# Optimization experiments

Hardware: AMD Instinct MI355X
Metric: run time of the kernel (lower is better)

The kernel has to match this reference:

```python
import jax, jax.numpy as jnp
import numpy as np

B, HS, WS = 4, 64, 64
UP = 8
H, W = HS * UP, WS * UP
C_ORI, C_MNT, C_OFF = 90, 180, 8
K = 1024            # max minutiae candidates per image (64*64 cells max 4096)
THRESH = 0.5
DIST_T = 16.0
ANG_T = np.pi / 6


def setup_inputs() -> dict:
    key = jax.random.key(0)
    ks = jax.random.split(key, 8)
    return {
        'segmentation': jax.random.uniform(ks[0], (B, 1, HS, WS), jnp.float32),
        'segmentation_up': jax.random.uniform(ks[1], (B, 1, H, W), jnp.float32),
        'orientation_up': jax.random.normal(ks[2], (B, C_ORI, H, W), jnp.float32),
        'enhanced_real': jax.random.normal(ks[3], (B, 1, H, W), jnp.float32),
        'minutiae_score': jax.random.uniform(ks[4], (B, 1, HS, WS), jnp.float32),
        'minutiae_orientation': jax.random.normal(ks[5], (B, C_MNT, HS, WS), jnp.float32),
        'minutiae_x_offset': jax.random.normal(ks[6], (B, C_OFF, HS, WS), jnp.float32),
        'minutiae_y_offset': jax.random.normal(ks[7], (B, C_OFF, HS, WS), jnp.float32),
    }


def _opening(x, k):
    # morphological opening (erosion then dilation) with a k x k ones kernel,
    # separable min/max pooling; geodesic border (pad so border is neutral).
    pl, pr = (k - 1) // 2, k // 2

    def pool(v, comp, init, pad_val):
        vp = jnp.pad(v, ((0, 0), (pl, pr), (pl, pr)), constant_values=pad_val)
        vp = jax.lax.reduce_window(vp, init, comp, (1, k, 1), (1, 1, 1), 'VALID')
        return jax.lax.reduce_window(vp, init, comp, (1, 1, k), (1, 1, 1), 'VALID')

    er = pool(x, jax.lax.min, np.inf, 1e4)
    return pool(er, jax.lax.max, -np.inf, -1e4)


def _nms_keep(xy, ang, valid):
    # xy: [K,2], ang: [K], valid: [K] bool; entries already sorted by score desc
    d = jnp.sqrt(jnp.sum((xy[:, None, :] - xy[None, :, :]) ** 2, axis=-1))
    da = jnp.abs(ang[:, None] - ang[None, :])
    da = jnp.minimum(da, 2 * jnp.pi - da)
    sup = (d < DIST_T) & (da < ANG_T) & valid[:, None] & valid[None, :]
    idxs = jnp.arange(K)

    def body(i, keep):
        return keep & ~(sup[i] & (idxs > i) & keep[i])

    return jax.lax.fori_loop(0, K, body, valid)


def _detect(score, ori, xo, yo):
    # score: [HS,WS]; ori: [C_MNT,HS,WS]; xo/yo: [C_OFF,HS,WS]
    h, w = score.shape
    flat = score.reshape(-1)
    masked = jnp.where(flat > THRESH, flat, -1.0)
    vals, idx = jax.lax.top_k(masked, K)          # sorted descending
    valid = vals > THRESH
    rows = idx // w
    cols = idx % w
    ang_idx = jnp.argmax(ori.reshape(C_MNT, -1)[:, idx], axis=0)
    xoff = jnp.argmax(xo.reshape(C_OFF, -1)[:, idx], axis=0)
    yoff = jnp.argmax(yo.reshape(C_OFF, -1)[:, idx], axis=0)
    angles = (ang_idx.astype(jnp.float32) * 2.0 - 89.0) * (np.pi / 180.0)
    xc = cols.astype(jnp.float32) * 8.0 + xoff.astype(jnp.float32)
    yc = rows.astype(jnp.float32) * 8.0 + yoff.astype(jnp.float32)
    scores = flat[idx]
    m = jnp.stack([xc, yc, angles, scores], axis=-1)  # [K,4]
    keep = _nms_keep(m[:, :2], angles, valid)
    return m, keep


def reference(segmentation, segmentation_up, orientation_up, enhanced_real,
              minutiae_score, minutiae_orientation, minutiae_x_offset,
              minutiae_y_offset):
    mask = _opening(jnp.round(segmentation[:, 0]), 5)          # [B,HS,WS]
    mask_up = _opening(jnp.round(segmentation_up[:, 0]), 5 * UP)  # [B,H,W]

    score = minutiae_score[:, 0] * mask
    minut, keep = jax.vmap(_detect)(score, minutiae_orientation,
                                    minutiae_x_offset, minutiae_y_offset)
    minut = minut * keep[..., None].astype(minut.dtype)       # zero suppressed

    ori_field = (jnp.argmax(orientation_up, axis=1).astype(jnp.float32) * 2.0
                 - 90.0) * (np.pi / 180.0) * mask_up

    enh = enhanced_real[:, 0] * mask_up
    ef = enh.reshape(B, -1)
    emin = ef.min(axis=1, keepdims=True)
    emax = ef.max(axis=1, keepdims=True)
    enh_vis = ((ef - emin) / (emax - emin + 1e-8)).reshape(B, H, W) * 255.0

    return (minut, keep.astype(jnp.float32), enh_vis, mask_up * 255.0, ori_field)
```

## Files before the change

### kernel.cpp

```cpp
#include <hip/hip_runtime.h>
#include <math.h>

#define Hh 512
#define Wh 512
#define Bn 4
#define C_ORIc 90
#define C_MNTc 180
#define C_OFFc 8
#define Kc 1024

#define O_MINUT 0
#define O_KEEP  (Bn*Kc*4)
#define O_VIS   (O_KEEP + Bn*Kc)
#define O_MASK  (O_VIS + Bn*Hh*Wh)
#define O_ORI   (O_MASK + Bn*Hh*Wh)

#define PI_180 0.017453292519943295f
#define TWO_PI 6.283185307179586f
#define ANG_T  0.5235987755982988f

#define IMG    262144
#define PB     (256*Bn)

__device__ __forceinline__ unsigned enc_f(float f) {
    unsigned u = __float_as_uint(f);
    return (u & 0x80000000u) ? ~u : (u | 0x80000000u);
}
__device__ __forceinline__ float dec_f(unsigned e) {
    return __uint_as_float((e & 0x80000000u) ? (e ^ 0x80000000u) : ~e);
}

template <bool ISMIN, bool BIN>
__device__ __forceinline__ void vert_pass_body(const float* __restrict__ in,
                                               float* __restrict__ outp, int blk)
{
    const float SENT = ISMIN ? 1e30f : -1e30f;
    int b  = blk >> 8;
    int rg = (blk >> 3) & 31;
    int cg = blk & 7;
    int tx = threadIdx.x & 63, ty = threadIdx.x >> 6;
    int c  = cg * 64 + tx;
    int r0 = rg * 16 + ty * 4;
    const float* p = in + (size_t)b * IMG + c;

    #define LDV(rr) (((rr) >= 0 && (rr) < 512) ? (BIN ? rintf(p[(rr) * 512]) \
                                                      : p[(rr) * 512]) : SENT)
    #define OPV(a, bb) (ISMIN ? fminf(a, bb) : fmaxf(a, bb))
    float core = SENT;
    #pragma unroll
    for (int k = 0; k < 37; k++) core = OPV(core, LDV(r0 - 16 + k));
    float L2v = LDV(r0 - 17);
    float L1v = OPV(LDV(r0 - 18), L2v);
    float L0v = OPV(LDV(r0 - 19), L1v);
    float H1v = LDV(r0 + 21);
    float H2v = OPV(H1v, LDV(r0 + 22));
    float H3v = OPV(H2v, LDV(r0 + 23));
    float* q = outp + (size_t)b * IMG + (size_t)r0 * 512 + c;
    q[0]    = OPV(core, L0v);
    q[512]  = OPV(core, OPV(L1v, H1v));
    q[1024] = OPV(core, OPV(L2v, H2v));
    q[1536] = OPV(core, H3v);
    #undef LDV
    #undef OPV
}

__global__ __launch_bounds__(256) void k1_vert_erode_detect(
    const float* __restrict__ segup, const float* __restrict__ mscore,
    const float* __restrict__ seg, const float* __restrict__ mo,
    const float* __restrict__ xo, const float* __restrict__ yo,
    float* __restrict__ out, float* __restrict__ T1, unsigned* __restrict__ mmu)
{
    __shared__ union {
        unsigned long long keys[4096];
        float scr[8320];
    } U;
    __shared__ unsigned smBits[128];
    __shared__ unsigned short smHalf[256];

    int tid = threadIdx.x;
    if (blockIdx.x < PB) {
        vert_pass_body<true, true>(segup, T1, blockIdx.x);
        return;
    }

    int b = blockIdx.x - PB;
    if (tid == 0) { mmu[b * 2] = 0xFFFFFFFFu; mmu[b * 2 + 1] = 0u; }

    const float* sg = seg + b * 4096;
    float* scr0 = U.scr;
    float* scr1 = U.scr + 4160;
    for (int i = tid; i < 4096; i += 256)
        scr0[(i >> 6) * 65 + (i & 63)] = rintf(sg[i]);
    __syncthreads();
    for (int i = tid; i < 4096; i += 256) {
        int r = i >> 6, c = i & 63;
        int lo = max(r - 2, 0), hi = min(r + 2, 63);
        float m = 1e30f;
        for (int rr = lo; rr <= hi; rr++) m = fminf(m, scr0[rr * 65 + c]);
        scr1[r * 65 + c] = m;
    }
    __syncthreads();
    for (int i = tid; i < 4096; i += 256) {
        int r = i >> 6, c = i & 63;
        int lo = max(c - 2, 0), hi = min(c + 2, 63);
        float m = 1e30f;
        for (int cc = lo; cc <= hi; cc++) m = fminf(m, scr1[r * 65 + cc]);
        scr0[r * 65 + c] = m;
    }
    __syncthreads();
    for (int i = tid; i < 4096; i += 256) {
        int r = i >> 6, c = i & 63;
        int lo = max(r - 2, 0), hi = min(r + 2, 63);
        float m = -1e30f;
        for (int rr = lo; rr <= hi; rr++) m = fmaxf(m, scr0[rr * 65 + c]);
        scr1[r * 65 + c] = m;
    }
    __syncthreads();
    {
        unsigned short bits16 = 0;
        int i0 = tid * 16;
        int r = i0 >> 6;
        for (int j = 0; j < 16; j++) {
            int c = (i0 + j) & 63;
            int lo = max(c - 2, 0), hi = min(c + 2, 63);
            float m = -1e30f;
            for (int cc = lo; cc <= hi; cc++) m = fmaxf(m, scr1[r * 65 + cc]);
            bits16 |= ((unsigned short)(m != 0.0f)) << j;
        }
        smHalf[tid] = bits16;
    }
    __syncthreads();
    if (tid < 128)
        smBits[tid] = (unsigned)smHalf[2 * tid] | ((unsigned)smHalf[2 * tid + 1] << 16);
    __syncthreads();

    const float* sp = mscore + b * 4096;
    bool anyv = false;
    for (int i = tid; i < 4096; i += 256) {
        unsigned m = (smBits[i >> 5] >> (i & 31)) & 1u;
        anyv |= (m && sp[i] > 0.5f);
    }
    if (!__syncthreads_or(anyv)) {
        float4 z = {0.f, 0.f, 0.f, 0.f};
        float4* mo4 = (float4*)(out + O_MINUT + (size_t)b * 4096);
        for (int i = tid; i < 1024; i += 256) mo4[i] = z;
        ((float4*)(out + O_KEEP + (size_t)b * 1024))[tid] = z;
        return;
    }

    for (int i = tid; i < 4096; i += 256) {
        unsigned m = (smBits[i >> 5] >> (i & 31)) & 1u;
        float s = m ? sp[i] : 0.0f;
        float mval = (s > 0.5f) ? s : -1.0f;
        unsigned fb = __float_as_uint(mval);
        unsigned od = (fb & 0x80000000u) ? ~fb : (fb | 0x80000000u);
        U.keys[i] = ((unsigned long long)(~od) << 32) | (unsigned)i;
    }
    for (int k = 2; k <= 4096; k <<= 1) {
        for (int j = k >> 1; j > 0; j >>= 1) {
            __syncthreads();
            for (int t = tid; t < 4096; t += 256) {
                int ixj = t ^ j;
                if (ixj > t) {
                    unsigned long long va = U.keys[t], vb = U.keys[ixj];
                    bool up = ((t & k) == 0);
                    if ((va > vb) == up) { U.keys[t] = vb; U.keys[ixj] = va; }
                }
            }
        }
    }
    __syncthreads();

    int idxs[4]; float ss[4]; int vld[4];
    int Nv = 0;
    for (int j = 0; j < 4; j++) {
        int slot = tid + j * 256;
        int idx = (int)(U.keys[slot] & 0xffffffffu);
        unsigned m = (smBits[idx >> 5] >> (idx & 31)) & 1u;
        float s = m ? sp[idx] : 0.0f;
        idxs[j] = idx; ss[j] = s; vld[j] = (s > 0.5f);
        Nv += __syncthreads_count(vld[j]);
    }

    float xcs[4], ycs[4], angs[4];
    for (int j = 0; j < 4; j++) {
        int slot = tid + j * 256;
        xcs[j] = ycs[j] = angs[j] = 0.f;
        if (slot < Nv) {
            int idx = idxs[j];
            int rr = idx >> 6, cc = idx & 63;
            const float* op_ = mo + (size_t)b * C_MNTc * 4096 + idx;
            float best = op_[0]; int bi = 0;
            for (int ch = 1; ch < C_MNTc; ch++) {
                float v = op_[ch * 4096];
                if (v > best) { best = v; bi = ch; }
            }
            const float* xp = xo + (size_t)b * C_OFFc * 4096 + idx;
            float bxv = xp[0]; int bx = 0;
            for (int ch = 1; ch < C_OFFc; ch++) {
                float v = xp[ch * 4096];
                if (v > bxv) { bxv = v; bx = ch; }
            }
            const float* yp = yo + (size_t)b * C_OFFc * 4096 + idx;
            float byv = yp[0]; int by = 0;
            for (int ch = 1; ch < C_OFFc; ch++) {
                float v = yp[ch * 4096];
                if (v > byv) { byv = v; by = ch; }
            }
            angs[j] = ((float)bi * 2.0f - 89.0f) * PI_180;
            xcs[j]  = (float)cc * 8.0f + (float)bx;
            ycs[j]  = (float)rr * 8.0f + (float)by;
        }
    }
    __syncthreads();
    float* sx = U.scr;
    float* sy = U.scr + 1024;
    float* sa = U.scr + 2048;
    int*   keep = (int*)(U.scr + 3072);
    for (int j = 0; j < 4; j++) {
        int slot = tid + j * 256;
        sx[slot] = xcs[j]; sy[slot] = ycs[j]; sa[slot] = angs[j];
        keep[slot] = (slot < Nv) ? 1 : 0;
    }
    __syncthreads();

    for (int i = 0; i < Nv; i++) {
        if (keep[i]) {
            float xi = sx[i], yi = sy[i], ai = sa[i];
            for (int j = 0; j < 4; j++) {
                int slot = tid + j * 256;
                if (slot > i && slot < Nv && keep[slot]) {
                    float dx = xcs[j] - xi, dy = ycs[j] - yi;
                    float d = sqrtf(dx * dx + dy * dy);
                    float da = fabsf(angs[j] - ai);
                    da = fminf(da, TWO_PI - da);
                    if (d < 16.0f && da < ANG_T) keep[slot] = 0;
                }
            }
        }
        __syncthreads();
    }
    for (int j = 0; j < 4; j++) {
        int slot = tid + j * 256;
        int kf = keep[slot];
        float* mout = out + O_MINUT + (size_t)b * 4096 + slot * 4;
        if (kf) {
            mout[0] = xcs[j]; mout[1] = ycs[j]; mout[2] = angs[j]; mout[3] = ss[j];
        } else {
            mout[0] = 0.f; mout[1] = 0.f; mout[2] = 0.f; mout[3] = 0.f;
        }
        out[O_KEEP + b * 1024 + slot] = (float)kf;
    }
}

__global__ __launch_bounds__(512) void k2_horiz_erode(const float* __restrict__ T1,
                                                      float* __restrict__ T2)
{
    __shared__ float row[4][512];
    int b = blockIdx.y;
    int r0 = blockIdx.x * 4;
    int tx = threadIdx.x, ty = threadIdx.y;
    const float* p = T1 + (size_t)b * IMG + (size_t)(r0 + ty) * 512;
    ((float4*)row[ty])[tx] = ((const float4*)p)[tx];
    __syncthreads();
    int c0 = tx * 4;
    const float* rw = row[ty];
    #define LDH(cc) (((cc) >= 0 && (cc) < 512) ? rw[cc] : 1e30f)
    float core = 1e30f;
    #pragma unroll
    for (int k = 0; k < 37; k++) core = fminf(core, LDH(c0 - 16 + k));
    float L2v = LDH(c0 - 17);
    float L1v = fminf(LDH(c0 - 18), L2v);
    float L0v = fminf(LDH(c0 - 19), L1v);
    float H1v = LDH(c0 + 21);
    float H2v = fminf(H1v, LDH(c0 + 22));
    float H3v = fminf(H2v, LDH(c0 + 23));
    #undef LDH
    float4 o;
    o.x = fminf(core, L0v);
    o.y = fminf(core, fminf(L1v, H1v));
    o.z = fminf(core, fminf(L2v, H2v));
    o.w = fminf(core, H3v);
    ((float4*)(T2 + (size_t)b * IMG + (size_t)(r0 + ty) * 512))[tx] = o;
}

__global__ __launch_bounds__(256) void k3_vert_dilate(const float* __restrict__ T2,
                                                      float* __restrict__ T3)
{
    vert_pass_body<false, false>(T2, T3, blockIdx.x);
}

__global__ __launch_bounds__(512) void k4_final(const float* __restrict__ T3,
                                                const float* __restrict__ ori,
                                                const float* __restrict__ enh,
                                                float* __restrict__ out,
                                                unsigned* __restrict__ mmu)
{
    __shared__ float row[4][512];
    __shared__ float red[512];
    int b = blockIdx.y;
    int r0 = blockIdx.x * 4;
    int tx = threadIdx.x, ty = threadIdx.y;
    int ltid = ty * 128 + tx;
    const float* p = T3 + (size_t)b * IMG + (size_t)(r0 + ty) * 512;
    ((float4*)row[ty])[tx] = ((const float4*)p)[tx];
    __syncthreads();
    int c0 = tx * 4;
    const float* rw = row[ty];
    #define LDD(cc) (((cc) >= 0 && (cc) < 512) ? rw[cc] : -1e30f)
    float core = -1e30f;
    #pragma unroll
    for (int k = 0; k < 37; k++) core = fmaxf(core, LDD(c0 - 16 + k));
    float L2v = LDD(c0 - 17);
    float L1v = fmaxf(LDD(c0 - 18), L2v);
    float L0v = fmaxf(LDD(c0 - 19), L1v);
    float H1v = LDD(c0 + 21);
    float H2v = fmaxf(H1v, LDD(c0 + 22));
    float H3v = fmaxf(H2v, LDD(c0 + 23));
    #undef LDD
    float m[4];
    m[0] = fmaxf(core, L0v);
    m[1] = fmaxf(core, fmaxf(L1v, H1v));
    m[2] = fmaxf(core, fmaxf(L2v, H2v));
    m[3] = fmaxf(core, H3v);

    size_t base = (size_t)b * IMG + (size_t)(r0 + ty) * 512 + c0;
    float4 mk = {m[0] * 255.f, m[1] * 255.f, m[2] * 255.f, m[3] * 255.f};
    *((float4*)(out + O_MASK + base)) = mk;

    float ov[4];
    for (int j = 0; j < 4; j++) {
        ov[j] = 0.0f;
        if (m[j] != 0.0f) {
            const float* op_ = ori + (size_t)b * C_ORIc * IMG
                             + (size_t)(r0 + ty) * 512 + (c0 + j);
            float best = op_[0];
            int bi = 0;
            for (int ch = 1; ch < C_ORIc; ch++) {
                float v = op_[(size_t)ch * IMG];
                if (v > best) { best = v; bi = ch; }
            }
            ov[j] = ((float)bi * 2.0f - 90.0f) * PI_180 * m[j];
        }
    }
    float4 o4 = {ov[0], ov[1], ov[2], ov[3]};
    *((float4*)(out + O_ORI + base)) = o4;

    float4 e4 = ((const float4*)(enh + (size_t)b * IMG + (size_t)(r0 + ty) * 512))[tx];
    float e0 = e4.x * m[0], e1 = e4.y * m[1], e2 = e4.z * m[2], e3 = e4.w * m[3];
    float lmin = fminf(fminf(e0, e1), fminf(e2, e3));
    float lmax = fmaxf(fmaxf(e0, e1), fmaxf(e2, e3));

    red[ltid] = lmin;
    __syncthreads();
    for (int s = 256; s > 0; s >>= 1) {
        if (ltid < s) red[ltid] = fminf(red[ltid], red[ltid + s]);
        __syncthreads();
    }
    float bmin = red[0];
    __syncthreads();
    red[ltid] = lmax;
    __syncthreads();
    for (int s = 256; s > 0; s >>= 1) {
        if (ltid < s) red[ltid] = fmaxf(red[ltid], red[ltid + s]);
        __syncthreads();
    }
    if (ltid == 0) {
        atomicMin(&mmu[b * 2 + 0], enc_f(bmin));
        atomicMax(&mmu[b * 2 + 1], enc_f(red[0]));
    }
}

__global__ __launch_bounds__(256) void k5_vis(const float* __restrict__ enh,
                                              const float* __restrict__ maskout,
                                              const unsigned* __restrict__ mmu,
                                              float* __restrict__ vis)
{
    int i4 = blockIdx.x * 256 + threadIdx.x;
    int b = i4 >> 16;
    float4 e = ((const float4*)enh)[i4];
    float4 mk = ((const float4*)maskout)[i4];
    float emin = dec_f(mmu[b * 2]);
    float den = dec_f(mmu[b * 2 + 1]) - emin + 1e-8f;
    float4 o;
    o.x = (e.x * (mk.x != 0.f ? 1.f : 0.f) - emin) / den * 255.0f;
    o.y = (e.y * (mk.y != 0.f ? 1.f : 0.f) - emin) / den * 255.0f;
    o.z = (e.z * (mk.z != 0.f ? 1.f : 0.f) - emin) / den * 255.0f;
    o.w = (e.w * (mk.w != 0.f ? 1.f : 0.f) - emin) / den * 255.0f;
    ((float4*)vis)[i4] = o;
}

extern "C" void kernel_launch(void* const* d_in, const int* in_sizes, int n_in,
                              void* d_out_, int out_size, void* d_ws, size_t ws_size,
                              hipStream_t stream)
{
    const float* seg    = (const float*)d_in[0];
    const float* segup  = (const float*)d_in[1];
    const float* oriup  = (const float*)d_in[2];
    const float* enh    = (const float*)d_in[3];
    const float* mscore = (const float*)d_in[4];
    const float* mori   = (const float*)d_in[5];
    const float* mxo    = (const float*)d_in[6];
    const float* myo    = (const float*)d_in[7];
    float* out = (float*)d_out_;

    unsigned* mmu = (unsigned*)d_ws;
    float* T1 = (float*)d_ws + 16;
    float* T2 = T1 + Bn * IMG;
    float* T3 = T2 + Bn * IMG;

    k1_vert_erode_detect<<<PB + Bn, 256, 0, stream>>>(segup, mscore, seg, mori,
                                                      mxo, myo, out, T1, mmu);
    k2_horiz_erode<<<dim3(128, Bn), dim3(128, 4), 0, stream>>>(T1, T2);
    k3_vert_dilate<<<PB, 256, 0, stream>>>(T2, T3);
    k4_final<<<dim3(128, Bn), dim3(128, 4), 0, stream>>>(T3, oriup, enh, out, mmu);
    k5_vis<<<(Bn * IMG) / 1024, 256, 0, stream>>>(enh, out + O_MASK, mmu,
                                                  out + O_VIS);
}
```

Baseline: 483.7 us.

## Fuse opening into tiled bit-packed morphology kernel, drop intermediate float buffers

Replaces the four-pass float erosion/dilation pipeline (vertical and horizontal min/max kernels writing full-size intermediates) with a single tiled kernel. Each 64x64 tile loads a haloed binarized block as ballot bitmasks and does the 40x40 opening with log-step AND/OR shifts in shared memory. The orientation argmax, mask output and per-tile enhanced min/max are computed in the same kernel. The vis kernel reads a packed mask bitmap and does the final min/max reduction itself, removing the atomics and the float mask reread. This cuts global traffic and kernel launches, but leaves only 260 blocks for the heavy 90-channel orientation argmax, which may lower occupancy.

```diff
diff --git a/kernel.cpp b/kernel.cpp
--- a/kernel.cpp
+++ b/kernel.cpp
@@ -1,393 +1,430 @@
 #include <hip/hip_runtime.h>
 #include <math.h>
 
-#define Hh 512
-#define Wh 512
 #define Bn 4
 #define C_ORIc 90
 #define C_MNTc 180
 #define C_OFFc 8
-#define Kc 1024
+#define IMG    262144
 
 #define O_MINUT 0
-#define O_KEEP  (Bn*Kc*4)
-#define O_VIS   (O_KEEP + Bn*Kc)
-#define O_MASK  (O_VIS + Bn*Hh*Wh)
-#define O_ORI   (O_MASK + Bn*Hh*Wh)
+#define O_KEEP  (Bn*1024*4)
+#define O_VIS   (O_KEEP + Bn*1024)
+#define O_MASK  (O_VIS + Bn*IMG)
+#define O_ORI   (O_MASK + Bn*IMG)
 
 #define PI_180 0.017453292519943295f
 #define TWO_PI 6.283185307179586f
 #define ANG_T  0.5235987755982988f
 
-#define IMG    262144
-#define PB     (256*Bn)
-
-__device__ __forceinline__ unsigned enc_f(float f) {
-    unsigned u = __float_as_uint(f);
-    return (u & 0x80000000u) ? ~u : (u | 0x80000000u);
-}
-__device__ __forceinline__ float dec_f(unsigned e) {
-    return __uint_as_float((e & 0x80000000u) ? (e ^ 0x80000000u) : ~e);
-}
-
-template <bool ISMIN, bool BIN>
-__device__ __forceinline__ void vert_pass_body(const float* __restrict__ in,
-                                               float* __restrict__ outp, int blk)
-{
-    const float SENT = ISMIN ? 1e30f : -1e30f;
-    int b  = blk >> 8;
-    int rg = (blk >> 3) & 31;
-    int cg = blk & 7;
-    int tx = threadIdx.x & 63, ty = threadIdx.x >> 6;
-    int c  = cg * 64 + tx;
-    int r0 = rg * 16 + ty * 4;
-    const float* p = in + (size_t)b * IMG + c;
-
-    #define LDV(rr) (((rr) >= 0 && (rr) < 512) ? (BIN ? rintf(p[(rr) * 512]) \
-                                                      : p[(rr) * 512]) : SENT)
-    #define OPV(a, bb) (ISMIN ? fminf(a, bb) : fmaxf(a, bb))
-    float core = SENT;
+__device__ __forceinline__ void h_and(unsigned* w, int k) {
+    unsigned t[7];
     #pragma unroll
-    for (int k = 0; k < 37; k++) core = OPV(core, LDV(r0 - 16 + k));
-    float L2v = LDV(r0 - 17);
-    float L1v = OPV(LDV(r0 - 18), L2v);
-    float L0v = OPV(LDV(r0 - 19), L1v);
-    float H1v = LDV(r0 + 21);
-    float H2v = OPV(H1v, LDV(r0 + 22));
-    float H3v = OPV(H2v, LDV(r0 + 23));
-    float* q = outp + (size_t)b * IMG + (size_t)r0 * 512 + c;
-    q[0]    = OPV(core, L0v);
-    q[512]  = OPV(core, OPV(L1v, H1v));
-    q[1024] = OPV(core, OPV(L2v, H2v));
-    q[1536] = OPV(core, H3v);
-    #undef LDV
-    #undef OPV
-}
-
-__global__ __launch_bounds__(256) void k1_vert_erode_detect(
-    const float* __restrict__ segup, const float* __restrict__ mscore,
-    const float* __restrict__ seg, const float* __restrict__ mo,
+    for (int i = 0; i < 7; i++) {
+        unsigned hi = (i < 6) ? w[i + 1] : 0xFFFFFFFFu;
+        t[i] = w[i] & ((w[i] >> k) | (hi << (32 - k)));
+    }
+    #pragma unroll
+    for (int i = 0; i < 7; i++) w[i] = t[i];
+}
+
+__device__ __forceinline__ void h_or(unsigned* w, int k) {
+    unsigned t[7];
+    #pragma unroll
+    for (int i = 0; i < 7; i++) {
+        unsigned hi = (i < 6) ? w[i + 1] : 0u;
+        t[i] = w[i] | ((w[i] >> k) | (hi << (32 - k)));
+    }
+    #pragma unroll
+    for (int i = 0; i < 7; i++) w[i] = t[i];
+}
+
+__device__ __forceinline__ unsigned rangemask(int lo, int hi, int base) {
+    int a = lo - base, b2 = hi - base;
+    if (a < 0) a = 0;
+    if (b2 > 31) b2 = 31;
+    if (a > b2) return 0u;
+    unsigned m = (b2 == 31) ? 0xFFFFFFFFu : ((1u << (b2 + 1)) - 1u);
+    return m & (0xFFFFFFFFu << a);
+}
+
+__global__ __launch_bounds__(256) void ka_main(
+    const float* __restrict__ segup, const float* __restrict__ seg,
+    const float* __restrict__ mscore, const float* __restrict__ mo,
     const float* __restrict__ xo, const float* __restrict__ yo,
-    float* __restrict__ out, float* __restrict__ T1, unsigned* __restrict__ mmu)
+    const float* __restrict__ ori, const float* __restrict__ enh,
+    float* __restrict__ out, float* __restrict__ ws)
 {
     __shared__ union {
         unsigned long long keys[4096];
         float scr[8320];
+        struct {
+            unsigned bb[4][852];
+            unsigned maskw[128];
+            float red[256];
+        } t;
     } U;
     __shared__ unsigned smBits[128];
     __shared__ unsigned short smHalf[256];
 
     int tid = threadIdx.x;
-    if (blockIdx.x < PB) {
-        vert_pass_body<true, true>(segup, T1, blockIdx.x);
+
+    if (blockIdx.x >= 256) {
+        int b = blockIdx.x - 256;
+
+        const float* sg = seg + b * 4096;
+        float* scr0 = U.scr;
+        float* scr1 = U.scr + 4160;
+        for (int i = tid; i < 4096; i += 256)
+            scr0[(i >> 6) * 65 + (i & 63)] = rintf(sg[i]);
+        __syncthreads();
+        for (int i = tid; i < 4096; i += 256) {
+            int r = i >> 6, c = i & 63;
+            int lo = max(r - 2, 0), hi = min(r + 2, 63);
+            float m = 1e30f;
+            for (int rr = lo; rr <= hi; rr++) m = fminf(m, scr0[rr * 65 + c]);
+            scr1[r * 65 + c] = m;
+        }
+        __syncthreads();
+        for (int i = tid; i < 4096; i += 256) {
+            int r = i >> 6, c = i & 63;
+            int lo = max(c - 2, 0), hi = min(c + 2, 63);
+            float m = 1e30f;
+            for (int cc = lo; cc <= hi; cc++) m = fminf(m, scr1[r * 65 + cc]);
+            scr0[r * 65 + c] = m;
+        }
+        __syncthreads();
+        for (int i = tid; i < 4096; i += 256) {
+            int r = i >> 6, c = i & 63;
+            int lo = max(r - 2, 0), hi = min(r + 2, 63);
+            float m = -1e30f;
+            for (int rr = lo; rr <= hi; rr++) m = fmaxf(m, scr0[rr * 65 + c]);
+            scr1[r * 65 + c] = m;
+        }
+        __syncthreads();
+        {
+            unsigned short bits16 = 0;
+            int i0 = tid * 16;
+            int r = i0 >> 6;
+            for (int j = 0; j < 16; j++) {
+                int c = (i0 + j) & 63;
+                int lo = max(c - 2, 0), hi = min(c + 2, 63);
+                float m = -1e30f;
+                for (int cc = lo; cc <= hi; cc++) m = fmaxf(m, scr1[r * 65 + cc]);
+                bits16 |= ((unsigned short)(m != 0.0f)) << j;
+            }
+            smHalf[tid] = bits16;
+        }
+        __syncthreads();
+        if (tid < 128)
+            smBits[tid] = (unsigned)smHalf[2 * tid] | ((unsigned)smHalf[2 * tid + 1] << 16);
+        __syncthreads();
+
+        const float* sp = mscore + b * 4096;
+        bool anyv = false;
+        for (int i = tid; i < 4096; i += 256) {
+            unsigned m = (smBits[i >> 5] >> (i & 31)) & 1u;
+            anyv |= (m && sp[i] > 0.5f);
+        }
+        if (!__syncthreads_or(anyv)) {
+            float4 z = {0.f, 0.f, 0.f, 0.f};
+            float4* mo4 = (float4*)(out + O_MINUT + (size_t)b * 4096);
+            for (int i = tid; i < 1024; i += 256) mo4[i] = z;
+            ((float4*)(out + O_KEEP + (size_t)b * 1024))[tid] = z;
+            return;
+        }
+
+        for (int i = tid; i < 4096; i += 256) {
+            unsigned m = (smBits[i >> 5] >> (i & 31)) & 1u;
+            float s = m ? sp[i] : 0.0f;
+            float mval = (s > 0.5f) ? s : -1.0f;
+            unsigned fb = __float_as_uint(mval);
+            unsigned od = (fb & 0x80000000u) ? ~fb : (fb | 0x80000000u);
+            U.keys[i] = ((unsigned long long)(~od) << 32) | (unsigned)i;
+        }
+        for (int k = 2; k <= 4096; k <<= 1) {
+            for (int j = k >> 1; j > 0; j >>= 1) {
+                __syncthreads();
+                for (int t = tid; t < 4096; t += 256) {
+                    int ixj = t ^ j;
+                    if (ixj > t) {
+                        unsigned long long va = U.keys[t], vb = U.keys[ixj];
+                        bool up = ((t & k) == 0);
+                        if ((va > vb) == up) { U.keys[t] = vb; U.keys[ixj] = va; }
+                    }
+                }
+            }
+        }
+        __syncthreads();
+
+        int idxs[4]; float ss[4]; int vld[4];
+        int Nv = 0;
+        for (int j = 0; j < 4; j++) {
+            int slot = tid + j * 256;
+            int idx = (int)(U.keys[slot] & 0xffffffffu);
+            unsigned m = (smBits[idx >> 5] >> (idx & 31)) & 1u;
+            float s = m ? sp[idx] : 0.0f;
+            idxs[j] = idx; ss[j] = s; vld[j] = (s > 0.5f);
+            Nv += __syncthreads_count(vld[j]);
+        }
+
+        float xcs[4], ycs[4], angs[4];
+        for (int j = 0; j < 4; j++) {
+            int slot = tid + j * 256;
+            xcs[j] = ycs[j] = angs[j] = 0.f;
+            if (slot < Nv) {
+                int idx = idxs[j];
+                int rr = idx >> 6, cc = idx & 63;
+                const float* op_ = mo + (size_t)b * C_MNTc * 4096 + idx;
+                float best = op_[0]; int bi = 0;
+                for (int ch = 1; ch < C_MNTc; ch++) {
+                    float v = op_[ch * 4096];
+                    if (v > best) { best = v; bi = ch; }
+                }
+                const float* xp = xo + (size_t)b * C_OFFc * 4096 + idx;
+                float bxv = xp[0]; int bx = 0;
+                for (int ch = 1; ch < C_OFFc; ch++) {
+                    float v = xp[ch * 4096];
+                    if (v > bxv) { bxv = v; bx = ch; }
+                }
+                const float* yp = yo + (size_t)b * C_OFFc * 4096 + idx;
+                float byv = yp[0]; int by = 0;
+                for (int ch = 1; ch < C_OFFc; ch++) {
+                    float v = yp[ch * 4096];
+                    if (v > byv) { byv = v; by = ch; }
+                }
+                angs[j] = ((float)bi * 2.0f - 89.0f) * PI_180;
+                xcs[j]  = (float)cc * 8.0f + (float)bx;
+                ycs[j]  = (float)rr * 8.0f + (float)by;
+            }
+        }
+        __syncthreads();
+        float* sx = U.scr;
+        float* sy = U.scr + 1024;
+        float* sa = U.scr + 2048;
+        int*   keep = (int*)(U.scr + 3072);
+        for (int j = 0; j < 4; j++) {
+            int slot = tid + j * 256;
+            sx[slot] = xcs[j]; sy[slot] = ycs[j]; sa[slot] = angs[j];
+            keep[slot] = (slot < Nv) ? 1 : 0;
+        }
+        __syncthreads();
+
+        for (int i = 0; i < Nv; i++) {
+            if (keep[i]) {
+                float xi = sx[i], yi = sy[i], ai = sa[i];
+                for (int j = 0; j < 4; j++) {
+                    int slot = tid + j * 256;
+                    if (slot > i && slot < Nv && keep[slot]) {
+                        float dx = xcs[j] - xi, dy = ycs[j] - yi;
+                        float d = sqrtf(dx * dx + dy * dy);
+                        float da = fabsf(angs[j] - ai);
+                        da = fminf(da, TWO_PI - da);
+                        if (d < 16.0f && da < ANG_T) keep[slot] = 0;
+                    }
+                }
+            }
+            __syncthreads();
+        }
+        for (int j = 0; j < 4; j++) {
+            int slot = tid + j * 256;
+            int kf = keep[slot];
+            float* mout = out + O_MINUT + (size_t)b * 4096 + slot * 4;
+            if (kf) {
+                mout[0] = xcs[j]; mout[1] = ycs[j]; mout[2] = angs[j]; mout[3] = ss[j];
+            } else {
+                mout[0] = 0.f; mout[1] = 0.f; mout[2] = 0.f; mout[3] = 0.f;
+            }
+            out[O_KEEP + b * 1024 + slot] = (float)kf;
+        }
         return;
     }
 
-    int b = blockIdx.x - PB;
-    if (tid == 0) { mmu[b * 2] = 0xFFFFFFFFu; mmu[b * 2 + 1] = 0u; }
-
-    const float* sg = seg + b * 4096;
-    float* scr0 = U.scr;
-    float* scr1 = U.scr + 4160;
-    for (int i = tid; i < 4096; i += 256)
-        scr0[(i >> 6) * 65 + (i & 63)] = rintf(sg[i]);
+    int b  = blockIdx.x >> 6;
+    int tt = blockIdx.x & 63;
+    int R0 = (tt >> 3) * 64;
+    int C0 = (tt & 7) * 64;
+
+    {
+        int wv = tid >> 6, lane = tid & 63;
+        const float* sup = segup + (size_t)b * IMG;
+        for (int r = wv; r < 142; r += 4) {
+            int gR = R0 - 38 + r;
+            bool rowin = ((unsigned)gR < 512u);
+            #pragma unroll
+            for (int sgi = 0; sgi < 3; sgi++) {
+                int lc = sgi * 64 + lane;
+                int gc = C0 - 38 + lc;
+                bool pred = true;
+                if (rowin && lc < 142 && gc >= 0 && gc < 512)
+                    pred = (rintf(sup[gR * 512 + gc]) != 0.0f);
+                unsigned long long bal = __ballot(pred);
+                if (lane == 0) {
+                    U.t.bb[0][r * 6 + sgi * 2]     = (unsigned)bal;
+                    U.t.bb[0][r * 6 + sgi * 2 + 1] = (unsigned)(bal >> 32);
+                }
+            }
+        }
+    }
     __syncthreads();
-    for (int i = tid; i < 4096; i += 256) {
-        int r = i >> 6, c = i & 63;
-        int lo = max(r - 2, 0), hi = min(r + 2, 63);
-        float m = 1e30f;
-        for (int rr = lo; rr <= hi; rr++) m = fminf(m, scr0[rr * 65 + c]);
-        scr1[r * 65 + c] = m;
+
+    #define VOP(DST, SRC, D, N, OPER)                                          \
+        for (int idx = tid; idx < (N) * 5; idx += 256) {                       \
+            int rr = idx / 5, wi = idx - rr * 5;                               \
+            U.t.bb[DST][rr * 6 + wi] =                                         \
+                U.t.bb[SRC][rr * 6 + wi] OPER U.t.bb[SRC][(rr + (D)) * 6 + wi];\
+        }                                                                      \
+        __syncthreads();
+
+    VOP(1, 0, 1, 141, &)
+    VOP(2, 1, 2, 139, &)
+    VOP(3, 2, 4, 135, &)
+    VOP(1, 3, 8, 127, &)
+    VOP(2, 1, 16, 111, &)
+    for (int idx = tid; idx < 103 * 5; idx += 256) {
+        int rr = idx / 5, wi = idx - rr * 5;
+        U.t.bb[0][rr * 6 + wi] = U.t.bb[2][rr * 6 + wi] & U.t.bb[3][(rr + 32) * 6 + wi];
     }
     __syncthreads();
-    for (int i = tid; i < 4096; i += 256) {
-        int r = i >> 6, c = i & 63;
-        int lo = max(c - 2, 0), hi = min(c + 2, 63);
-        float m = 1e30f;
-        for (int cc = lo; cc <= hi; cc++) m = fminf(m, scr1[r * 65 + cc]);
-        scr0[r * 65 + c] = m;
+
+    if (tid < 103) {
+        unsigned w[7], s8[7];
+        #pragma unroll
+        for (int i = 0; i < 5; i++) w[i] = U.t.bb[0][tid * 6 + i];
+        w[5] = w[6] = 0xFFFFFFFFu;
+        h_and(w, 1); h_and(w, 2); h_and(w, 4);
+        #pragma unroll
+        for (int i = 0; i < 7; i++) s8[i] = w[i];
+        h_and(w, 8); h_and(w, 16);
+        unsigned res[5];
+        #pragma unroll
+        for (int i = 0; i < 5; i++) res[i] = w[i] & s8[i + 1];
+        bool rowok = ((unsigned)(R0 - 19 + tid) < 512u);
+        int lo = 19 - C0;  if (lo < 0) lo = 0;
+        int hi = 531 - C0; if (hi > 102) hi = 102;
+        #pragma unroll
+        for (int i = 0; i < 5; i++) {
+            unsigned cm = rangemask(lo, hi, i * 32);
+            U.t.bb[1][tid * 6 + i] = rowok ? (res[i] & cm) : 0u;
+        }
     }
     __syncthreads();
-    for (int i = tid; i < 4096; i += 256) {
-        int r = i >> 6, c = i & 63;
-        int lo = max(r - 2, 0), hi = min(r + 2, 63);
-        float m = -1e30f;
-        for (int rr = lo; rr <= hi; rr++) m = fmaxf(m, scr0[rr * 65 + c]);
-        scr1[r * 65 + c] = m;
+
+    VOP(2, 1, 1, 102, |)
+    VOP(0, 2, 2, 100, |)
+    VOP(3, 0, 4, 96, |)
+    VOP(2, 3, 8, 88, |)
+    VOP(0, 2, 16, 72, |)
+    for (int idx = tid; idx < 64 * 5; idx += 256) {
+        int rr = idx / 5, wi = idx - rr * 5;
+        U.t.bb[1][rr * 6 + wi] = U.t.bb[0][rr * 6 + wi] | U.t.bb[3][(rr + 32) * 6 + wi];
     }
     __syncthreads();
+    #undef VOP
+
+    unsigned* wsbits = (unsigned*)(ws + 512);
+    if (tid < 64) {
+        unsigned w[7], s8[7];
+        #pragma unroll
+        for (int i = 0; i < 5; i++) w[i] = U.t.bb[1][tid * 6 + i];
+        w[5] = w[6] = 0u;
+        h_or(w, 1); h_or(w, 2); h_or(w, 4);
+        #pragma unroll
+        for (int i = 0; i < 7; i++) s8[i] = w[i];
+        h_or(w, 8); h_or(w, 16);
+        unsigned m0 = w[0] | s8[1];
+        unsigned m1 = w[1] | s8[2];
+        U.t.maskw[tid * 2]     = m0;
+        U.t.maskw[tid * 2 + 1] = m1;
+        size_t bro = ((size_t)b * 512 + R0 + tid) * 16 + (C0 >> 5);
+        wsbits[bro]     = m0;
+        wsbits[bro + 1] = m1;
+    }
+    __syncthreads();
+
     {
-        unsigned short bits16 = 0;
-        int i0 = tid * 16;
-        int r = i0 >> 6;
-        for (int j = 0; j < 16; j++) {
-            int c = (i0 + j) & 63;
-            int lo = max(c - 2, 0), hi = min(c + 2, 63);
-            float m = -1e30f;
-            for (int cc = lo; cc <= hi; cc++) m = fmaxf(m, scr1[r * 65 + cc]);
-            bits16 |= ((unsigned short)(m != 0.0f)) << j;
-        }
-        smHalf[tid] = bits16;
-    }
-    __syncthreads();
-    if (tid < 128)
-        smBits[tid] = (unsigned)smHalf[2 * tid] | ((unsigned)smHalf[2 * tid + 1] << 16);
-    __syncthreads();
-
-    const float* sp = mscore + b * 4096;
-    bool anyv = false;
-    for (int i = tid; i < 4096; i += 256) {
-        unsigned m = (smBits[i >> 5] >> (i & 31)) & 1u;
-        anyv |= (m && sp[i] > 0.5f);
-    }
-    if (!__syncthreads_or(anyv)) {
-        float4 z = {0.f, 0.f, 0.f, 0.f};
-        float4* mo4 = (float4*)(out + O_MINUT + (size_t)b * 4096);
-        for (int i = tid; i < 1024; i += 256) mo4[i] = z;
-        ((float4*)(out + O_KEEP + (size_t)b * 1024))[tid] = z;
-        return;
-    }
-
-    for (int i = tid; i < 4096; i += 256) {
-        unsigned m = (smBits[i >> 5] >> (i & 31)) & 1u;
-        float s = m ? sp[i] : 0.0f;
-        float mval = (s > 0.5f) ? s : -1.0f;
-        unsigned fb = __float_as_uint(mval);
-        unsigned od = (fb & 0x80000000u) ? ~fb : (fb | 0x80000000u);
-        U.keys[i] = ((unsigned long long)(~od) << 32) | (unsigned)i;
-    }
-    for (int k = 2; k <= 4096; k <<= 1) {
-        for (int j = k >> 1; j > 0; j >>= 1) {
+        int r  = tid >> 2;
+        int cg = (tid & 3) * 16;
+        unsigned w0 = U.t.maskw[r * 2], w1 = U.t.maskw[r * 2 + 1];
+        size_t base = (size_t)b * IMG + (size_t)(R0 + r) * 512 + C0 + cg;
+        float lmin = 1e30f, lmax = -1e30f;
+        for (int q = 0; q < 4; q++) {
+            int c = cg + q * 4;
+            float4 e = *((const float4*)(enh + base + q * 4));
+            float mf[4], ov[4];
+            #pragma unroll
+            for (int j = 0; j < 4; j++) {
+                int cc = c + j;
+                unsigned bit = (((cc < 32) ? w0 : w1) >> (cc & 31)) & 1u;
+                mf[j] = bit ? 1.0f : 0.0f;
+                ov[j] = 0.0f;
+                if (bit) {
+                    const float* op_ = ori + (size_t)b * C_ORIc * IMG
+                                     + (size_t)(R0 + r) * 512 + (C0 + cc);
+                    float best = op_[0]; int bi = 0;
+                    for (int ch = 1; ch < C_ORIc; ch++) {
+                        float v = op_[(size_t)ch * IMG];
+                        if (v > best) { best = v; bi = ch; }
+                    }
+                    ov[j] = ((float)bi * 2.0f - 90.0f) * PI_180 * mf[j];
+                }
+            }
+            float4 mk = {mf[0] * 255.f, mf[1] * 255.f, mf[2] * 255.f, mf[3] * 255.f};
+            *((float4*)(out + O_MASK + base + q * 4)) = mk;
+            float4 o4 = {ov[0], ov[1], ov[2], ov[3]};
+            *((float4*)(out + O_ORI + base + q * 4)) = o4;
+            float e0 = e.x * mf[0], e1 = e.y * mf[1], e2 = e.z * mf[2], e3 = e.w * mf[3];
+            lmin = fminf(lmin, fminf(fminf(e0, e1), fminf(e2, e3)));
+            lmax = fmaxf(lmax, fmaxf(fmaxf(e0, e1), fmaxf(e2, e3)));
+        }
+        U.t.red[tid] = lmin;
+        __syncthreads();
+        for (int s = 128; s > 0; s >>= 1) {
+            if (tid < s) U.t.red[tid] = fminf(U.t.red[tid], U.t.red[tid + s]);
             __syncthreads();
-            for (int t = tid; t < 4096; t += 256) {
-                int ixj = t ^ j;
-                if (ixj > t) {
-                    unsigned long long va = U.keys[t], vb = U.keys[ixj];
-                    bool up = ((t & k) == 0);
-                    if ((va > vb) == up) { U.keys[t] = vb; U.keys[ixj] = va; }
-                }
-            }
-        }
-    }
-    __syncthreads();
-
-    int idxs[4]; float ss[4]; int vld[4];
-    int Nv = 0;
-    for (int j = 0; j < 4; j++) {
-        int slot = tid + j * 256;
-        int idx = (int)(U.keys[slot] & 0xffffffffu);
-        unsigned m = (smBits[idx >> 5] >> (idx & 31)) & 1u;
-        float s = m ? sp[idx] : 0.0f;
-        idxs[j] = idx; ss[j] = s; vld[j] = (s > 0.5f);
-        Nv += __syncthreads_count(vld[j]);
-    }
-
-    float xcs[4], ycs[4], angs[4];
-    for (int j = 0; j < 4; j++) {
-        int slot = tid + j * 256;
-        xcs[j] = ycs[j] = angs[j] = 0.f;
-        if (slot < Nv) {
-            int idx = idxs[j];
-            int rr = idx >> 6, cc = idx & 63;
-            const float* op_ = mo + (size_t)b * C_MNTc * 4096 + idx;
-            float best = op_[0]; int bi = 0;
-            for (int ch = 1; ch < C_MNTc; ch++) {
-                float v = op_[ch * 4096];
-                if (v > best) { best = v; bi = ch; }
-            }
-            const float* xp = xo + (size_t)b * C_OFFc * 4096 + idx;
-            float bxv = xp[0]; int bx = 0;
-            for (int ch = 1; ch < C_OFFc; ch++) {
-                float v = xp[ch * 4096];
-                if (v > bxv) { bxv = v; bx = ch; }
-            }
-            const float* yp = yo + (size_t)b * C_OFFc * 4096 + idx;
-            float byv = yp[0]; int by = 0;
-            for (int ch = 1; ch < C_OFFc; ch++) {
-                float v = yp[ch * 4096];
-                if (v > byv) { byv = v; by = ch; }
-            }
-            angs[j] = ((float)bi * 2.0f - 89.0f) * PI_180;
-            xcs[j]  = (float)cc * 8.0f + (float)bx;
-            ycs[j]  = (float)rr * 8.0f + (float)by;
-        }
-    }
-    __syncthreads();
-    float* sx = U.scr;
-    float* sy = U.scr + 1024;
-    float* sa = U.scr + 2048;
-    int*   keep = (int*)(U.scr + 3072);
-    for (int j = 0; j < 4; j++) {
-        int slot = tid + j * 256;
-        sx[slot] = xcs[j]; sy[slot] = ycs[j]; sa[slot] = angs[j];
-        keep[slot] = (slot < Nv) ? 1 : 0;
-    }
-    __syncthreads();
-
-    for (int i = 0; i < Nv; i++) {
-        if (keep[i]) {
-            float xi = sx[i], yi = sy[i], ai = sa[i];
-            for (int j = 0; j < 4; j++) {
-                int slot = tid + j * 256;
-                if (slot > i && slot < Nv && keep[slot]) {
-                    float dx = xcs[j] - xi, dy = ycs[j] - yi;
-                    float d = sqrtf(dx * dx + dy * dy);
-                    float da = fabsf(angs[j] - ai);
-                    da = fminf(da, TWO_PI - da);
-                    if (d < 16.0f && da < ANG_T) keep[slot] = 0;
-                }
-            }
-        }
-        __syncthreads();
-    }
-    for (int j = 0; j < 4; j++) {
-        int slot = tid + j * 256;
-        int kf = keep[slot];
-        float* mout = out + O_MINUT + (size_t)b * 4096 + slot * 4;
-        if (kf) {
-            mout[0] = xcs[j]; mout[1] = ycs[j]; mout[2] = angs[j]; mout[3] = ss[j];
-        } else {
-            mout[0] = 0.f; mout[1] = 0.f; mout[2] = 0.f; mout[3] = 0.f;
-        }
-        out[O_KEEP + b * 1024 + slot] = (float)kf;
-    }
-}
-
-__global__ __launch_bounds__(512) void k2_horiz_erode(const float* __restrict__ T1,
-                                                      float* __restrict__ T2)
-{
-    __shared__ float row[4][512];
-    int b = blockIdx.y;
-    int r0 = blockIdx.x * 4;
-    int tx = threadIdx.x, ty = threadIdx.y;
-    const float* p = T1 + (size_t)b * IMG + (size_t)(r0 + ty) * 512;
-    ((float4*)row[ty])[tx] = ((const float4*)p)[tx];
-    __syncthreads();
-    int c0 = tx * 4;
-    const float* rw = row[ty];
-    #define LDH(cc) (((cc) >= 0 && (cc) < 512) ? rw[cc] : 1e30f)
-    float core = 1e30f;
-    #pragma unroll
-    for (int k = 0; k < 37; k++) core = fminf(core, LDH(c0 - 16 + k));
-    float L2v = LDH(c0 - 17);
-    float L1v = fminf(LDH(c0 - 18), L2v);
-    float L0v = fminf(LDH(c0 - 19), L1v);
-    float H1v = LDH(c0 + 21);
-    float H2v = fminf(H1v, LDH(c0 + 22));
-    float H3v = fminf(H2v, LDH(c0 + 23));
-    #undef LDH
-    float4 o;
-    o.x = fminf(core, L0v);
-    o.y = fminf(core, fminf(L1v, H1v));
-    o.z = fminf(core, fminf(L2v, H2v));
-    o.w = fminf(core, H3v);
-    ((float4*)(T2 + (size_t)b * IMG + (size_t)(r0 + ty) * 512))[tx] = o;
-}
-
-__global__ __launch_bounds__(256) void k3_vert_dilate(const float* __restrict__ T2,
-                                                      float* __restrict__ T3)
-{
-    vert_pass_body<false, false>(T2, T3, blockIdx.x);
-}
-
-__global__ __launch_bounds__(512) void k4_final(const float* __restrict__ T3,
-                                                const float* __restrict__ ori,
-                                                const float* __restrict__ enh,
-                                                float* __restrict__ out,
-                                                unsigned* __restrict__ mmu)
-{
-    __shared__ float row[4][512];
-    __shared__ float red[512];
-    int b = blockIdx.y;
-    int r0 = blockIdx.x * 4;
-    int tx = threadIdx.x, ty = threadIdx.y;
-    int ltid = ty * 128 + tx;
-    const float* p = T3 + (size_t)b * IMG + (size_t)(r0 + ty) * 512;
-    ((float4*)row[ty])[tx] = ((const float4*)p)[tx];
-    __syncthreads();
-    int c0 = tx * 4;
-    const float* rw = row[ty];
-    #define LDD(cc) (((cc) >= 0 && (cc) < 512) ? rw[cc] : -1e30f)
-    float core = -1e30f;
-    #pragma unroll
-    for (int k = 0; k < 37; k++) core = fmaxf(core, LDD(c0 - 16 + k));
-    float L2v = LDD(c0 - 17);
-    float L1v = fmaxf(LDD(c0 - 18), L2v);
-    float L0v = fmaxf(LDD(c0 - 19), L1v);
-    float H1v = LDD(c0 + 21);
-    float H2v = fmaxf(H1v, LDD(c0 + 22));
-    float H3v = fmaxf(H2v, LDD(c0 + 23));
-    #undef LDD
-    float m[4];
-    m[0] = fmaxf(core, L0v);
-    m[1] = fmaxf(core, fmaxf(L1v, H1v));
-    m[2] = fmaxf(core, fmaxf(L2v, H2v));
-    m[3] = fmaxf(core, H3v);
-
-    size_t base = (size_t)b * IMG + (size_t)(r0 + ty) * 512 + c0;
-    float4 mk = {m[0] * 255.f, m[1] * 255.f, m[2] * 255.f, m[3] * 255.f};
-    *((float4*)(out + O_MASK + base)) = mk;
-
-    float ov[4];
-    for (int j = 0; j < 4; j++) {
-        ov[j] = 0.0f;
-        if (m[j] != 0.0f) {
-            const float* op_ = ori + (size_t)b * C_ORIc * IMG
-                             + (size_t)(r0 + ty) * 512 + (c0 + j);
-            float best = op_[0];
-            int bi = 0;
-            for (int ch = 1; ch < C_ORIc; ch++) {
-                float v = op_[(size_t)ch * IMG];
-                if (v > best) { best = v; bi = ch; }
-            }
-            ov[j] = ((float)bi * 2.0f - 90.0f) * PI_180 * m[j];
-        }
-    }
-    float4 o4 = {ov[0], ov[1], ov[2], ov[3]};
-    *((float4*)(out + O_ORI + base)) = o4;
-
-    float4 e4 = ((const float4*)(enh + (size_t)b * IMG + (size_t)(r0 + ty) * 512))[tx];
-    float e0 = e4.x * m[0], e1 = e4.y * m[1], e2 = e4.z * m[2], e3 = e4.w * m[3];
-    float lmin = fminf(fminf(e0, e1), fminf(e2, e3));
-    float lmax = fmaxf(fmaxf(e0, e1), fmaxf(e2, e3));
-
-    red[ltid] = lmin;
-    __syncthreads();
-    for (int s = 256; s > 0; s >>= 1) {
-        if (ltid < s) red[ltid] = fminf(red[ltid], red[ltid + s]);
-        __syncthreads();
-    }
-    float bmin = red[0];
-    __syncthreads();
-    red[ltid] = lmax;
-    __syncthreads();
-    for (int s = 256; s > 0; s >>= 1) {
-        if (ltid < s) red[ltid] = fmaxf(red[ltid], red[ltid + s]);
-        __syncthreads();
-    }
-    if (ltid == 0) {
-        atomicMin(&mmu[b * 2 + 0], enc_f(bmin));
-        atomicMax(&mmu[b * 2 + 1], enc_f(red[0]));
-    }
-}
-
-__global__ __launch_bounds__(256) void k5_vis(const float* __restrict__ enh,
-                                              const float* __restrict__ maskout,
-                                              const unsigned* __restrict__ mmu,
-                                              float* __restrict__ vis)
+        }
+        float bmn = U.t.red[0];
+        __syncthreads();
+        U.t.red[tid] = lmax;
+        __syncthreads();
+        for (int s = 128; s > 0; s >>= 1) {
+            if (tid < s) U.t.red[tid] = fmaxf(U.t.red[tid], U.t.red[tid + s]);
+            __syncthreads();
+        }
+        if (tid == 0) {
+            ws[b * 64 + tt]       = bmn;
+            ws[256 + b * 64 + tt] = U.t.red[0];
+        }
+    }
+}
+
+__global__ __launch_bounds__(256) void kb_vis(const float* __restrict__ enh,
+                                              const float* __restrict__ ws,
+                                              float* __restrict__ out)
 {
     int i4 = blockIdx.x * 256 + threadIdx.x;
     int b = i4 >> 16;
+    int lane = threadIdx.x & 63;
+    float vmin = ws[b * 64 + lane];
+    float vmax = ws[256 + b * 64 + lane];
+    #pragma unroll
+    for (int off = 32; off > 0; off >>= 1) {
+        vmin = fminf(vmin, __shfl_xor(vmin, off));
+        vmax = fmaxf(vmax, __shfl_xor(vmax, off));
+    }
+    float den = vmax - vmin + 1e-8f;
+    const unsigned* bits = (const unsigned*)(ws + 512);
+    int p = (i4 & 65535) * 4;
+    int row = p >> 9, col = p & 511;
+    unsigned wv = bits[((size_t)b * 512 + row) * 16 + (col >> 5)];
+    unsigned sh = col & 31;
     float4 e = ((const float4*)enh)[i4];
-    float4 mk = ((const float4*)maskout)[i4];
-    float emin = dec_f(mmu[b * 2]);
-    float den = dec_f(mmu[b * 2 + 1]) - emin + 1e-8f;
     float4 o;
-    o.x = (e.x * (mk.x != 0.f ? 1.f : 0.f) - emin) / den * 255.0f;
-    o.y = (e.y * (mk.y != 0.f ? 1.f : 0.f) - emin) / den * 255.0f;
-    o.z = (e.z * (mk.z != 0.f ? 1.f : 0.f) - emin) / den * 255.0f;
-    o.w = (e.w * (mk.w != 0.f ? 1.f : 0.f) - emin) / den * 255.0f;
-    ((float4*)vis)[i4] = o;
+    o.x = (e.x * (((wv >> (sh + 0)) & 1u) ? 1.f : 0.f) - vmin) / den * 255.0f;
+    o.y = (e.y * (((wv >> (sh + 1)) & 1u) ? 1.f : 0.f) - vmin) / den * 255.0f;
+    o.z = (e.z * (((wv >> (sh + 2)) & 1u) ? 1.f : 0.f) - vmin) / den * 255.0f;
+    o.w = (e.w * (((wv >> (sh + 3)) & 1u) ? 1.f : 0.f) - vmin) / den * 255.0f;
+    ((float4*)(out + O_VIS))[i4] = o;
 }
 
 extern "C" void kernel_launch(void* const* d_in, const int* in_sizes, int n_in,
@@ -404,16 +441,9 @@
     const float* myo    = (const float*)d_in[7];
     float* out = (float*)d_out_;
 
-    unsigned* mmu = (unsigned*)d_ws;
-    float* T1 = (float*)d_ws + 16;
-    float* T2 = T1 + Bn * IMG;
-    float* T3 = T2 + Bn * IMG;
-
-    k1_vert_erode_detect<<<PB + Bn, 256, 0, stream>>>(segup, mscore, seg, mori,
-                                                      mxo, myo, out, T1, mmu);
-    k2_horiz_erode<<<dim3(128, Bn), dim3(128, 4), 0, stream>>>(T1, T2);
-    k3_vert_dilate<<<PB, 256, 0, stream>>>(T2, T3);
-    k4_final<<<dim3(128, Bn), dim3(128, 4), 0, stream>>>(T3, oriup, enh, out, mmu);
-    k5_vis<<<(Bn * IMG) / 1024, 256, 0, stream>>>(enh, out + O_MASK, mmu,
-                                                  out + O_VIS);
-}
+    float* ws = (float*)d_ws;
+
+    ka_main<<<260, 256, 0, stream>>>(segup, seg, mscore, mori, mxo, myo,
+                                     oriup, enh, out, ws);
+    kb_vis<<<1024, 256, 0, stream>>>(enh, ws, out);
+}
```

Result: faster. 464.0 us (-4.1%).
